# Kernel optimization log

Hardware: AMD Instinct MI355X
Metric: run time of the kernel (lower is better)

The kernel has to match this reference:

```python
import jax, jax.numpy as jnp
import numpy as np

HIDDEN = 64

def setup_inputs() -> dict:
    key = jax.random.key(0)
    ks = jax.random.split(key, 8)
    B, T, D, O, H = 1024, 256, 128, 128, HIDDEN
    s_ih = 1.0 / np.sqrt(H)
    inp = {
        "x": jax.random.normal(ks[0], (B, T, D), dtype=jnp.float32),
        "W_ih": jax.random.uniform(ks[1], (4 * H, D), jnp.float32, -s_ih, s_ih),
        "W_hh": jax.random.uniform(ks[2], (4 * H, H), jnp.float32, -s_ih, s_ih),
        "b_ih": jax.random.uniform(ks[3], (4 * H,), jnp.float32, -s_ih, s_ih),
        "b_hh": jax.random.uniform(ks[4], (4 * H,), jnp.float32, -s_ih, s_ih),
        "W_o": jax.random.uniform(ks[5], (O, H), jnp.float32, -s_ih, s_ih),
        "b_o": jax.random.uniform(ks[6], (O,), jnp.float32, -s_ih, s_ih),
    }
    return inp

def _lstm_last_h(x, W_ih, W_hh, b_ih, b_hh):
    # x: [B, T, D]. PyTorch gate order: i, f, g, o.
    B, T, D = x.shape
    H = HIDDEN
    # Precompute input contribution for all steps: [T, B, 4H]
    gx = jnp.einsum('btd,gd->tbg', x, W_ih) + (b_ih + b_hh)

    def step(carry, gx_t):
        h, c = carry
        gates = gx_t + h @ W_hh.T  # [B, 4H]
        i = jax.nn.sigmoid(gates[:, 0 * H:1 * H])
        f = jax.nn.sigmoid(gates[:, 1 * H:2 * H])
        g = jnp.tanh(gates[:, 2 * H:3 * H])
        o = jax.nn.sigmoid(gates[:, 3 * H:4 * H])
        c = f * c + i * g
        h = o * jnp.tanh(c)
        return (h, c), None

    h0 = jnp.zeros((B, H), x.dtype)
    c0 = jnp.zeros((B, H), x.dtype)
    (h_T, _), _ = jax.lax.scan(step, (h0, c0), gx)
    return h_T  # [B, H] == output[:, -1, :]

def reference(x, W_ih, W_hh, b_ih, b_hh, W_o, b_o):
    h = _lstm_last_h(x, W_ih, W_hh, b_ih, b_hh)
    logits = jax.nn.relu(h) @ W_o.T + b_o  # [B, O]; dropout is identity in eval
    return jax.nn.log_softmax(logits, axis=1)
```

## Files before the change

kernel.cpp:

```cpp
#include <hip/hip_runtime.h>
#include <math.h>

constexpr int B = 1024, T = 256, D = 128, H = 64, O = 128;
constexpr int BQ = 4;
constexpr int NBLK = B / BQ;
constexpr int TC = 8;
constexpr int NCH = T / TC;

typedef __attribute__((ext_vector_type(8))) short short8;
typedef __attribute__((ext_vector_type(4))) float f32x4;

__device__ __forceinline__ unsigned short f2bf(float f) {
    union { float f; unsigned u; } v; v.f = f;
    return (unsigned short)((v.u + 0x7FFF + ((v.u >> 16) & 1)) >> 16);
}
__device__ __forceinline__ float frcp(float x) { return __builtin_amdgcn_rcpf(x); }
__device__ __forceinline__ float sigmoidf_(float x) {
    return frcp(1.0f + __expf(-x));
}
__device__ __forceinline__ float tanhf_(float x) {
    return fmaf(2.0f, frcp(1.0f + __expf(-2.0f * x)), -1.0f);
}
__device__ __forceinline__ void lds_barrier() {
    asm volatile("s_waitcnt lgkmcnt(0)\n\ts_barrier" ::: "memory");
}

__global__ __launch_bounds__(256, 1)
void lstm_fused(const float* __restrict__ x, const float* __restrict__ Wih,
                const float* __restrict__ Whh, const float* __restrict__ bih,
                const float* __restrict__ bhh, const float* __restrict__ Wo,
                const float* __restrict__ bo, float* __restrict__ out)
{
    __shared__ unsigned short xfrag[2 * 2048];
    __shared__ unsigned short hfrag[2 * 1152];
    __shared__ float gbw[4 * 4 * 16 * 4];
    __shared__ float gxw[4 * 4 * 2 * 64 * 4];
    __shared__ float hfin[4 * 64];

    const int tid  = threadIdx.x;
    const int lane = tid & 63;
    const int w    = tid >> 6;
    const int lq   = lane & 15;
    const int qd   = lane >> 4;
    const int b0   = blockIdx.x * BQ;

    short8 wih_f[4][4];
    short8 whh_f[4][2];
    float  bias[4];
    #pragma unroll
    for (int q = 0; q < 4; ++q) {
        const int n = 64 * q + 16 * w + lq;
        #pragma unroll
        for (int c = 0; c < 4; ++c) {
            const float* p = Wih + (size_t)n * D + 32 * c + 8 * qd;
            short8 v;
            #pragma unroll
            for (int j = 0; j < 8; ++j) v[j] = (short)f2bf(p[j]);
            wih_f[q][c] = v;
        }
        #pragma unroll
        for (int c = 0; c < 2; ++c) {
            const float* p = Whh + (size_t)n * H + 32 * c + 8 * qd;
            short8 v;
            #pragma unroll
            for (int j = 0; j < 8; ++j) v[j] = (short)f2bf(p[j]);
            whh_f[q][c] = v;
        }
        bias[q] = bih[n] + bhh[n];
    }

    const int ms    = tid >> 4;
    const int kslot = tid & 15;
    const int c_p   = kslot >> 2;
    const int q_p   = kslot & 3;
    const int l_p   = (q_p << 4) | ms;
    const int xoff  = c_p * 1024 + ((l_p * 16) ^ (c_p * 32));
    const int bb    = ms & 3, tsp = ms >> 2;
    const float* xbase = x + (size_t)(b0 + bb) * T * D + 8 * kslot;

    int xro[4];
    #pragma unroll
    for (int c = 0; c < 4; ++c) xro[c] = c * 1024 + ((lane * 16) ^ (c * 32));

    for (int i = tid; i < 1152; i += 256) ((unsigned int*)hfrag)[i] = 0;

    float4 pf[2][2];

    #pragma unroll
    for (int g = 0; g < 2; ++g) {
        const float* p = xbase + (size_t)(4 * g + tsp) * D;
        pf[g][0] = *(const float4*)p;
        pf[g][1] = *(const float4*)(p + 4);
    }
    #pragma unroll
    for (int g = 0; g < 2; ++g) {
        float4 a = pf[g][0], bv = pf[g][1];
        short8 v;
        v[0] = (short)f2bf(a.x);  v[1] = (short)f2bf(a.y);
        v[2] = (short)f2bf(a.z);  v[3] = (short)f2bf(a.w);
        v[4] = (short)f2bf(bv.x); v[5] = (short)f2bf(bv.y);
        v[6] = (short)f2bf(bv.z); v[7] = (short)f2bf(bv.w);
        *(short8*)((char*)xfrag + g * 4096 + xoff) = v;
    }
    #pragma unroll
    for (int g = 0; g < 2; ++g) {
        const float* p = xbase + (size_t)(TC + 4 * g + tsp) * D;
        pf[g][0] = *(const float4*)p;
        pf[g][1] = *(const float4*)(p + 4);
    }
    __syncthreads();

    float gxr[TC][4];

    auto gx_burst = [&]() {
        #pragma unroll
        for (int g = 0; g < 2; ++g) {
            short8 xf[4];
            #pragma unroll
            for (int c = 0; c < 4; ++c)
                xf[c] = *(const short8*)((char*)xfrag + g * 4096 + xro[c]);
            #pragma unroll
            for (int q = 0; q < 4; ++q) {
                f32x4 a = {bias[q], bias[q], bias[q], bias[q]};
                #pragma unroll
                for (int c = 0; c < 4; ++c)
                    a = __builtin_amdgcn_mfma_f32_16x16x32_bf16(xf[c], wih_f[q][c], a, 0, 0, 0);
                *(f32x4*)&gxw[(((w * 4 + q) * 2 + g) * 64 + lane) * 4] = a;
            }
        }
        #pragma unroll
        for (int tt = 0; tt < TC; ++tt)
            #pragma unroll
            for (int q = 0; q < 4; ++q)
                gxr[tt][q] = gxw[(((w * 4 + q) * 2 + (tt >> 2)) * 64 +
                                  (((tt & 3) << 4) | lq)) * 4 + qd];
    };

    gx_burst();
    lds_barrier();
    #pragma unroll
    for (int g = 0; g < 2; ++g) {
        float4 a = pf[g][0], bv = pf[g][1];
        short8 v;
        v[0] = (short)f2bf(a.x);  v[1] = (short)f2bf(a.y);
        v[2] = (short)f2bf(a.z);  v[3] = (short)f2bf(a.w);
        v[4] = (short)f2bf(bv.x); v[5] = (short)f2bf(bv.y);
        v[6] = (short)f2bf(bv.z); v[7] = (short)f2bf(bv.w);
        *(short8*)((char*)xfrag + g * 4096 + xoff) = v;
    }
    #pragma unroll
    for (int g = 0; g < 2; ++g) {
        const float* p = xbase + (size_t)(2 * TC + 4 * g + tsp) * D;
        pf[g][0] = *(const float4*)p;
        pf[g][1] = *(const float4*)(p + 4);
    }

    float cst = 0.0f, hlast = 0.0f;

    for (int ch = 0; ch < NCH; ++ch) {
        #pragma unroll
        for (int tt = 0; tt < TC; ++tt) {
            const int hcur = tt & 1, hnxt = hcur ^ 1;

            short8 hfr[2];
            #pragma unroll
            for (int c = 0; c < 2; ++c)
                hfr[c] = *(const short8*)((char*)hfrag + hcur * 2304 +
                                          lq * 144 + c * 64 + qd * 16);
            f32x4 acc[4];
            #pragma unroll
            for (int q = 0; q < 4; ++q) {
                f32x4 a = {0.f, 0.f, 0.f, 0.f};
                #pragma unroll
                for (int c = 0; c < 2; ++c)
                    a = __builtin_amdgcn_mfma_f32_16x16x32_bf16(hfr[c], whh_f[q][c], a, 0, 0, 0);
                acc[q] = a;
            }

            if (lane < 16) {
                #pragma unroll
                for (int q = 0; q < 4; ++q)
                    *(f32x4*)&gbw[((w * 4 + q) * 16 + lane) * 4] = acc[q];
            }
            float gi = sigmoidf_(gbw[((w * 4 + 0) * 16 + lq) * 4 + qd] + gxr[tt][0]);
            float gf = sigmoidf_(gbw[((w * 4 + 1) * 16 + lq) * 4 + qd] + gxr[tt][1]);
            float gg = tanhf_  (gbw[((w * 4 + 2) * 16 + lq) * 4 + qd] + gxr[tt][2]);
            float go = sigmoidf_(gbw[((w * 4 + 3) * 16 + lq) * 4 + qd] + gxr[tt][3]);
            float c2 = fmaf(gf, cst, gi * gg);
            cst = c2;
            float hv = go * tanhf_(c2);
            hlast = hv;
            hfrag[hnxt * 1152 + qd * 72 + 16 * w + lq] = f2bf(hv);

            lds_barrier();
        }

        if (ch + 1 < NCH) {
            gx_burst();
            lds_barrier();
            #pragma unroll
            for (int g = 0; g < 2; ++g) {
                float4 a = pf[g][0], bv = pf[g][1];
                short8 v;
                v[0] = (short)f2bf(a.x);  v[1] = (short)f2bf(a.y);
                v[2] = (short)f2bf(a.z);  v[3] = (short)f2bf(a.w);
                v[4] = (short)f2bf(bv.x); v[5] = (short)f2bf(bv.y);
                v[6] = (short)f2bf(bv.z); v[7] = (short)f2bf(bv.w);
                *(short8*)((char*)xfrag + g * 4096 + xoff) = v;
            }
            const int ch3 = (ch + 3 < NCH) ? ch + 3 : NCH - 1;
            #pragma unroll
            for (int g = 0; g < 2; ++g) {
                const float* p = xbase + ((size_t)ch3 * TC + 4 * g + tsp) * D;
                pf[g][0] = *(const float4*)p;
                pf[g][1] = *(const float4*)(p + 4);
            }
        }
    }

    hfin[qd * 64 + 16 * w + lq] = hlast;
    __syncthreads();

    {
        const int m = w;
        float l0 = bo[lane], l1 = bo[lane + 64];
        const float* w0 = Wo + (size_t)lane * H;
        const float* w1 = Wo + (size_t)(lane + 64) * H;
        #pragma unroll
        for (int k = 0; k < H; ++k) {
            float rh = fmaxf(hfin[m * 64 + k], 0.0f);
            l0 += rh * w0[k];
            l1 += rh * w1[k];
        }
        float mx = fmaxf(l0, l1);
        #pragma unroll
        for (int sh = 32; sh > 0; sh >>= 1) mx = fmaxf(mx, __shfl_xor(mx, sh));
        float e = __expf(l0 - mx) + __expf(l1 - mx);
        #pragma unroll
        for (int sh = 32; sh > 0; sh >>= 1) e += __shfl_xor(e, sh);
        float lse = mx + __logf(e);
        float* op = out + (size_t)(b0 + m) * O;
        op[lane]      = l0 - lse;
        op[lane + 64] = l1 - lse;
    }
}

extern "C" void kernel_launch(void* const* d_in, const int* in_sizes, int n_in,
                              void* d_out, int out_size, void* d_ws, size_t ws_size,
                              hipStream_t stream) {
    const float* x   = (const float*)d_in[0];
    const float* Wih = (const float*)d_in[1];
    const float* Whh = (const float*)d_in[2];
    const float* bih = (const float*)d_in[3];
    const float* bhh = (const float*)d_in[4];
    const float* Wo  = (const float*)d_in[5];
    const float* bo  = (const float*)d_in[6];
    lstm_fused<<<dim3(NBLK), dim3(256), 0, stream>>>(
        x, Wih, Whh, bih, bhh, Wo, bo, (float*)d_out);
}
```

Before: 286.0 us.

## Keep LSTM gate precompute in registers and shrink h fragment layout

```diff
diff --git a/kernel.cpp b/kernel.cpp
--- a/kernel.cpp
+++ b/kernel.cpp
@@ -32,9 +32,7 @@
                 const float* __restrict__ bo, float* __restrict__ out)
 {
     __shared__ unsigned short xfrag[2 * 2048];
-    __shared__ unsigned short hfrag[2 * 1152];
-    __shared__ float gbw[4 * 4 * 16 * 4];
-    __shared__ float gxw[4 * 4 * 2 * 64 * 4];
+    __shared__ unsigned short hfrag[2 * 4 * 96];
     __shared__ float hfin[4 * 64];
 
     const int tid  = threadIdx.x;
@@ -75,14 +73,14 @@
     const int q_p   = kslot & 3;
     const int l_p   = (q_p << 4) | ms;
     const int xoff  = c_p * 1024 + ((l_p * 16) ^ (c_p * 32));
-    const int bb    = ms & 3, tsp = ms >> 2;
+    const int bb    = ms >> 2, tsp = ms & 3;
     const float* xbase = x + (size_t)(b0 + bb) * T * D + 8 * kslot;
 
     int xro[4];
     #pragma unroll
     for (int c = 0; c < 4; ++c) xro[c] = c * 1024 + ((lane * 16) ^ (c * 32));
 
-    for (int i = tid; i < 1152; i += 256) ((unsigned int*)hfrag)[i] = 0;
+    for (int i = tid; i < 384; i += 256) ((unsigned int*)hfrag)[i] = 0;
 
     float4 pf[2][2];
 
@@ -125,15 +123,10 @@
                 #pragma unroll
                 for (int c = 0; c < 4; ++c)
                     a = __builtin_amdgcn_mfma_f32_16x16x32_bf16(xf[c], wih_f[q][c], a, 0, 0, 0);
-                *(f32x4*)&gxw[(((w * 4 + q) * 2 + g) * 64 + lane) * 4] = a;
-            }
-        }
-        #pragma unroll
-        for (int tt = 0; tt < TC; ++tt)
-            #pragma unroll
-            for (int q = 0; q < 4; ++q)
-                gxr[tt][q] = gxw[(((w * 4 + q) * 2 + (tt >> 2)) * 64 +
-                                  (((tt & 3) << 4) | lq)) * 4 + qd];
+                #pragma unroll
+                for (int r = 0; r < 4; ++r) gxr[4 * g + r][q] = a[r];
+            }
+        }
     };
 
     gx_burst();
@@ -165,32 +158,28 @@
             short8 hfr[2];
             #pragma unroll
             for (int c = 0; c < 2; ++c)
-                hfr[c] = *(const short8*)((char*)hfrag + hcur * 2304 +
-                                          lq * 144 + c * 64 + qd * 16);
-            f32x4 acc[4];
+                hfr[c] = *(const short8*)(hfrag + hcur * 384 +
+                                          (lq >> 2) * 96 + 32 * c + 8 * qd);
+
+            float gv[4];
             #pragma unroll
             for (int q = 0; q < 4; ++q) {
-                f32x4 a = {0.f, 0.f, 0.f, 0.f};
+                f32x4 a = {gxr[tt][q], 0.0f, 0.0f, 0.0f};
                 #pragma unroll
                 for (int c = 0; c < 2; ++c)
                     a = __builtin_amdgcn_mfma_f32_16x16x32_bf16(hfr[c], whh_f[q][c], a, 0, 0, 0);
-                acc[q] = a;
-            }
-
-            if (lane < 16) {
-                #pragma unroll
-                for (int q = 0; q < 4; ++q)
-                    *(f32x4*)&gbw[((w * 4 + q) * 16 + lane) * 4] = acc[q];
-            }
-            float gi = sigmoidf_(gbw[((w * 4 + 0) * 16 + lq) * 4 + qd] + gxr[tt][0]);
-            float gf = sigmoidf_(gbw[((w * 4 + 1) * 16 + lq) * 4 + qd] + gxr[tt][1]);
-            float gg = tanhf_  (gbw[((w * 4 + 2) * 16 + lq) * 4 + qd] + gxr[tt][2]);
-            float go = sigmoidf_(gbw[((w * 4 + 3) * 16 + lq) * 4 + qd] + gxr[tt][3]);
+                gv[q] = a[0];
+            }
+
+            float gi = sigmoidf_(gv[0]);
+            float gf = sigmoidf_(gv[1]);
+            float gg = tanhf_  (gv[2]);
+            float go = sigmoidf_(gv[3]);
             float c2 = fmaf(gf, cst, gi * gg);
             cst = c2;
             float hv = go * tanhf_(c2);
             hlast = hv;
-            hfrag[hnxt * 1152 + qd * 72 + 16 * w + lq] = f2bf(hv);
+            hfrag[hnxt * 384 + qd * 96 + 16 * w + lq] = f2bf(hv);
 
             lds_barrier();
         }
```

Result: slower. 297.7 us (+4.1%).
